# Performance work log

Measured on AMD Instinct MI355X. Metric: run time of the kernel, lower is better.

The kernel has to match this reference:

```python
import jax, jax.numpy as jnp
import numpy as np

P = 3            # spline degree
N_KNOTS = 68     # len(t); K = N_KNOTS - P - 1 = 64
B, D_IN, D_OUT = 4096, 256, 256


def bspline_basis(u, t, p):
    """Vectorized Cox-de Boor recursion.
    u: (N,) evaluation points; t: (n,) sorted knot vector.
    Returns (N, n - p - 1) basis matrix.
    """
    n = t.shape[0]
    uu = u[:, None]                                   # (N, 1)
    # degree-0 indicators over half-open knot intervals: (N, n-1)
    Bmat = ((uu >= t[None, :-1]) & (uu < t[None, 1:])).astype(u.dtype)
    for d in range(1, p + 1):
        ld = t[d:n - 1] - t[:n - d - 1]               # (n-d-1,) left denominators
        rd = t[d + 1:] - t[1:n - d]                   # (n-d-1,) right denominators
        lt = jnp.where(ld > 0, (uu - t[None, :n - d - 1]) / jnp.where(ld > 0, ld, 1.0), 0.0)
        rt = jnp.where(rd > 0, (t[None, d + 1:] - uu) / jnp.where(rd > 0, rd, 1.0), 0.0)
        Bmat = lt * Bmat[:, :-1] + rt * Bmat[:, 1:]
    return Bmat                                        # (N, K)


def setup_inputs() -> dict:
    key = jax.random.key(0)
    k1, k2 = jax.random.split(key)
    K = N_KNOTS - P - 1
    x = jax.random.normal(k1, (B, D_IN), dtype=jnp.float32)
    coeffs = 0.01 * jax.random.normal(k2, (D_OUT, D_IN, K), dtype=jnp.float32)
    mask = jnp.ones((D_OUT, D_IN), dtype=jnp.float32)
    t = jnp.linspace(-4.0, 4.0, N_KNOTS, dtype=jnp.float32)
    return {"x": x, "coeffs": coeffs, "mask": mask, "t": t}


def reference(x, coeffs, mask, t):
    b, d_in = x.shape
    # basis for all (batch, input-dim) points at once -> (B, d_in, K)
    Bx = bspline_basis(x.reshape(-1), t, P).reshape(b, d_in, -1)
    C = coeffs * mask[..., None]                      # (d_out, d_in, K)
    y = jnp.einsum('bik,oik->bo', Bx, C)              # (B, d_out)
    return y
```

## Files before the change

kernel.cpp:

```cpp
#include <hip/hip_runtime.h>

#define NKNOTS 68
#define B_     4096
#define DIN    256
#define DOUT   256
#define KB_    64
#define BM     128
#define BN     128
#define LDT    72
#define KSPLIT 16
#define IPS    (DIN / KSPLIT)

typedef unsigned short ushort_t;
typedef __bf16 bf16_t;
typedef bf16_t  bf16x8   __attribute__((ext_vector_type(8)));
typedef float   f32x4    __attribute__((ext_vector_type(4)));
typedef unsigned int u32x4 __attribute__((ext_vector_type(4)));
typedef ushort_t us16x4  __attribute__((ext_vector_type(4)));

typedef __attribute__((address_space(1))) const unsigned int gu32;
typedef __attribute__((address_space(3))) unsigned int lu32;

__device__ __forceinline__ float bf2f(ushort_t b) {
    union { unsigned u; float f; } c; c.u = ((unsigned)b) << 16; return c.f;
}
__device__ __forceinline__ ushort_t f2bf(float f) {
    union { float f; unsigned u; } c; c.f = f;
    unsigned u = c.u;
    return (ushort_t)((u + 0x7FFFu + ((u >> 16) & 1u)) >> 16);
}
__device__ __forceinline__ bool is_fp32(const void* tkn) {
    return ((*(const unsigned*)tkn) & 0xFFFFu) == 0u;
}

__global__ void kan_prep(const void* __restrict__ coeffs,
                         const void* __restrict__ mask,
                         const void* __restrict__ x,
                         const void* __restrict__ tkn,
                         ushort_t* __restrict__ cp,
                         ushort_t* __restrict__ basis4,
                         unsigned char* __restrict__ span) {
    __shared__ float tt[NKNOTS];
    int blk = blockIdx.x;
    int lt  = threadIdx.x;
    bool f32 = is_fp32(tkn);

    if (blk < 2048) {
        int tid = blk * 256 + lt;
        int oi = tid >> 3;
        int k8 = (tid & 7) * 8;
        size_t base = (size_t)oi * KB_ + k8;
        float v[8], m;
        if (f32) {
            const float* cf = (const float*)coeffs + base;
            f32x4 a = *(const f32x4*)cf;
            f32x4 b = *(const f32x4*)(cf + 4);
            v[0]=a.x; v[1]=a.y; v[2]=a.z; v[3]=a.w; v[4]=b.x; v[5]=b.y; v[6]=b.z; v[7]=b.w;
            m = ((const float*)mask)[oi];
        } else {
            const ushort_t* ch = (const ushort_t*)coeffs + base;
            u32x4 w = *(const u32x4*)ch;
            const ushort_t* h = (const ushort_t*)&w;
            #pragma unroll
            for (int e = 0; e < 8; ++e) v[e] = bf2f(h[e]);
            m = bf2f(((const ushort_t*)mask)[oi]);
        }
        us16x4 o0v, o1v;
        #pragma unroll
        for (int e = 0; e < 4; ++e) o0v[e] = f2bf(v[e] * m);
        #pragma unroll
        for (int e = 0; e < 4; ++e) o1v[e] = f2bf(v[4 + e] * m);
        *(us16x4*)(cp + base)     = o0v;
        *(us16x4*)(cp + base + 4) = o1v;
    } else {
        if (lt < NKNOTS) tt[lt] = f32 ? ((const float*)tkn)[lt] : bf2f(((const ushort_t*)tkn)[lt]);
        __syncthreads();
        int g = (blk - 2048) * 256 + lt;
        float u = f32 ? ((const float*)x)[g] : bf2f(((const ushort_t*)x)[g]);
        float N0 = 0.f, N1 = 0.f, N2 = 0.f, N3 = 0.f;
        int j = 0;
        bool valid = (u >= tt[0]) && (u < tt[NKNOTS - 1]);
        if (valid) {
            int lo = 0, hi = NKNOTS - 1;
            #pragma unroll
            for (int it = 0; it < 7; ++it) {
                int mid = (lo + hi) >> 1;
                if (u < tt[mid]) hi = mid; else lo = mid;
            }
            j = lo;
            float Nv[4];
            Nv[0] = 1.f; Nv[1] = 0.f; Nv[2] = 0.f; Nv[3] = 0.f;
            #pragma unroll
            for (int d = 1; d <= 3; ++d) {
                float saved = 0.f;
                #pragma unroll
                for (int r = 0; r < 3; ++r) {
                    if (r < d) {
                        int il = j + r + 1 - d;
                        int ir = j + r + 1;
                        il = il < 0 ? 0 : (il > 67 ? 67 : il);
                        ir = ir > 67 ? 67 : ir;
                        float tl = tt[il], tr = tt[ir];
                        float denom = tr - tl;
                        float temp = (denom > 0.f) ? Nv[r] / denom : 0.f;
                        Nv[r] = saved + (tr - u) * temp;
                        saved = (u - tl) * temp;
                    }
                }
                Nv[d] = saved;
            }
            N0 = Nv[0]; N1 = Nv[1]; N2 = Nv[2]; N3 = Nv[3];
        }
        int s = j - 3;
        int sc = s < 0 ? 0 : (s > 60 ? 60 : s);
        us16x4 o4;
        #pragma unroll
        for (int r = 0; r < 4; ++r) {
            int rr = (sc + r) - s;
            float v = 0.f;
            v = (rr == 0) ? N0 : v;
            v = (rr == 1) ? N1 : v;
            v = (rr == 2) ? N2 : v;
            v = (rr == 3) ? N3 : v;
            o4[r] = f2bf(v);
        }
        ((us16x4*)basis4)[g] = o4;
        span[g] = (unsigned char)sc;
    }
}

__global__ __launch_bounds__(256, 4) void kan_gemm(
    const ushort_t* __restrict__ cp,
    const ushort_t* __restrict__ basis4,
    const unsigned char* __restrict__ span,
    ushort_t* __restrict__ part)
{
    __shared__ __align__(16) ushort_t As[BM * LDT];
    __shared__ __align__(16) ushort_t Bs[BM * KB_];

    int t  = threadIdx.x;
    int bx = blockIdx.x;
    int kt = bx & (KSPLIT - 1);
    int mt = (bx >> 4) & 31;
    int nt = bx >> 9;
    int b0 = mt * BM;
    int o0 = nt * BN;
    int i0 = kt * IPS;

    int wave = t >> 6;
    int lane = t & 63;
    int wm = (wave & 1) * 64;
    int wn = (wave >> 1) * 64;
    int l15 = lane & 15;
    int l4  = lane >> 4;

    {
        unsigned* As32 = (unsigned*)As;
        #pragma unroll
        for (int j = 0; j < (BM * LDT / 2) / 256; ++j) As32[t + j * 256] = 0u;
    }
    __syncthreads();

    f32x4 acc[4][4];
    #pragma unroll
    for (int a = 0; a < 4; ++a)
        #pragma unroll
        for (int b = 0; b < 4; ++b)
            acc[a][b] = (f32x4){0.f, 0.f, 0.f, 0.f};

    int zrow = t >> 2;
    int zq   = t & 3;
    int last0 = 0, last1 = 0;

    for (int ii = 0; ii < IPS; ++ii) {
        int i = i0 + ii;
        size_t gi0 = (size_t)(b0 + zrow) * DIN + i;
        size_t gi1 = (size_t)(b0 + zrow + 64) * DIN + i;
        int s0 = span[gi0];
        int s1 = span[gi1];
        ushort_t bv0 = basis4[gi0 * 4 + zq];
        ushort_t bv1 = basis4[gi1 * 4 + zq];
        #pragma unroll
        for (int j = 0; j < 4; ++j) {
            int slot = wave * 256 + j * 64 + lane;
            int row  = slot >> 3;
            int c    = (slot & 7) ^ (row & 7);
            const ushort_t* g = cp + ((size_t)(o0 + row) * DIN + i) * KB_ + c * 8;
            lu32* l = (lu32*)(Bs + (wave * 256 + j * 64) * 8);
            __builtin_amdgcn_global_load_lds((gu32*)g, l, 16, 0, 0);
        }
        As[zrow * LDT + last0 + zq] = 0;
        As[(zrow + 64) * LDT + last1 + zq] = 0;
        As[zrow * LDT + s0 + zq] = bv0;
        As[(zrow + 64) * LDT + s1 + zq] = bv1;
        last0 = s0; last1 = s1;
        __syncthreads();
        #pragma unroll
        for (int ks = 0; ks < 2; ++ks) {
            bf16x8 af[4], bfr[4];
            #pragma unroll
            for (int a = 0; a < 4; ++a)
                af[a] = *(const bf16x8*)(As + (wm + a * 16 + l15) * LDT + ks * 32 + l4 * 8);
            #pragma unroll
            for (int b = 0; b < 4; ++b) {
                int brow = wn + b * 16 + l15;
                int c2 = (ks * 4 + l4) ^ (brow & 7);
                bfr[b] = *(const bf16x8*)(Bs + brow * KB_ + c2 * 8);
            }
            #pragma unroll
            for (int a = 0; a < 4; ++a)
                #pragma unroll
                for (int b = 0; b < 4; ++b)
                    acc[a][b] = __builtin_amdgcn_mfma_f32_16x16x32_bf16(af[a], bfr[b], acc[a][b], 0, 0, 0);
        }
        __syncthreads();
    }
    ushort_t* pout = part + (size_t)kt * (B_ * DOUT);
    #pragma unroll
    for (int a = 0; a < 4; ++a) {
        int row_base = b0 + wm + a * 16 + l4 * 4;
        #pragma unroll
        for (int b = 0; b < 4; ++b) {
            int col = o0 + wn + b * 16 + l15;
            #pragma unroll
            for (int e = 0; e < 4; ++e)
                pout[(size_t)(row_base + e) * DOUT + col] = f2bf(acc[a][b][e]);
        }
    }
}

__global__ void kan_reduce(const ushort_t* __restrict__ part,
                           const void* __restrict__ tkn,
                           void* __restrict__ out) {
    int g = blockIdx.x * 256 + threadIdx.x;
    const us16x4* p4 = (const us16x4*)part;
    f32x4 s = (f32x4){0.f, 0.f, 0.f, 0.f};
    #pragma unroll
    for (int kt = 0; kt < KSPLIT; ++kt) {
        us16x4 v = p4[(size_t)kt * (B_ * DOUT / 4) + g];
        s.x += bf2f(v[0]); s.y += bf2f(v[1]); s.z += bf2f(v[2]); s.w += bf2f(v[3]);
    }
    if (is_fp32(tkn)) {
        ((f32x4*)out)[g] = s;
    } else {
        us16x4 o;
        o[0] = f2bf(s.x); o[1] = f2bf(s.y); o[2] = f2bf(s.z); o[3] = f2bf(s.w);
        ((us16x4*)out)[g] = o;
    }
}

extern "C" void kernel_launch(void* const* d_in, const int* in_sizes, int n_in,
                              void* d_out, int out_size, void* d_ws, size_t ws_size,
                              hipStream_t stream) {
    const void* x      = d_in[0];
    const void* coeffs = d_in[1];
    const void* mask   = d_in[2];
    const void* tkn    = d_in[3];

    char* ws = (char*)d_ws;
    ushort_t* cp            = (ushort_t*)(ws);
    ushort_t* basis4        = (ushort_t*)(ws + (8u  << 20));
    unsigned char* spanbuf  = (unsigned char*)(ws + (16u << 20));
    ushort_t* part          = (ushort_t*)(ws + (17u << 20));

    kan_prep<<<6144, 256, 0, stream>>>(coeffs, mask, x, tkn, cp, basis4, spanbuf);
    kan_gemm<<<1024, 256, 0, stream>>>(cp, basis4, spanbuf, part);
    kan_reduce<<<1024, 256, 0, stream>>>(part, tkn, d_out);
}
```

Measured before the change: 118.6 us.

## Quantize GEMM operands to int8 with per-output scaling and double-buffer coefficient tiles

Coefficients are quantized to int8 with a per-output-row absmax scale, computed by a new reduction pass using atomicMax. Basis values become int8 and are packed with the span index into a single 64-bit record. The GEMM switches to i32 int8 MFMA with K=64 per instruction and double-buffers the LDS coefficient tile so the next load overlaps the current compute. This halves operand bandwidth and MFMA count but adds an extra prep kernel plus a memset, and the int8 quantization may lose accuracy.

```diff
diff --git a/kernel.cpp b/kernel.cpp
--- a/kernel.cpp
+++ b/kernel.cpp
@@ -7,16 +7,16 @@
 #define KB_    64
 #define BM     128
 #define BN     128
-#define LDT    72
+#define LDA    80
 #define KSPLIT 16
 #define IPS    (DIN / KSPLIT)
 
 typedef unsigned short ushort_t;
-typedef __bf16 bf16_t;
-typedef bf16_t  bf16x8   __attribute__((ext_vector_type(8)));
+typedef unsigned long long u64_t;
 typedef float   f32x4    __attribute__((ext_vector_type(4)));
 typedef unsigned int u32x4 __attribute__((ext_vector_type(4)));
 typedef ushort_t us16x4  __attribute__((ext_vector_type(4)));
+typedef int     int4v    __attribute__((ext_vector_type(4)));
 
 typedef __attribute__((address_space(1))) const unsigned int gu32;
 typedef __attribute__((address_space(3))) unsigned int lu32;
@@ -33,14 +33,14 @@
     return ((*(const unsigned*)tkn) & 0xFFFFu) == 0u;
 }
 
-__global__ void kan_prep(const void* __restrict__ coeffs,
-                         const void* __restrict__ mask,
-                         const void* __restrict__ x,
-                         const void* __restrict__ tkn,
-                         ushort_t* __restrict__ cp,
-                         ushort_t* __restrict__ basis4,
-                         unsigned char* __restrict__ span) {
+__global__ void kan_prep1(const void* __restrict__ coeffs,
+                          const void* __restrict__ mask,
+                          const void* __restrict__ x,
+                          const void* __restrict__ tkn,
+                          unsigned* __restrict__ smax,
+                          u64_t* __restrict__ rec64) {
     __shared__ float tt[NKNOTS];
+    __shared__ float wmax[4];
     int blk = blockIdx.x;
     int lt  = threadIdx.x;
     bool f32 = is_fp32(tkn);
@@ -48,6 +48,7 @@
     if (blk < 2048) {
         int tid = blk * 256 + lt;
         int oi = tid >> 3;
+        int o  = tid >> 11;
         int k8 = (tid & 7) * 8;
         size_t base = (size_t)oi * KB_ + k8;
         float v[8], m;
@@ -65,13 +66,18 @@
             for (int e = 0; e < 8; ++e) v[e] = bf2f(h[e]);
             m = bf2f(((const ushort_t*)mask)[oi]);
         }
-        us16x4 o0v, o1v;
-        #pragma unroll
-        for (int e = 0; e < 4; ++e) o0v[e] = f2bf(v[e] * m);
-        #pragma unroll
-        for (int e = 0; e < 4; ++e) o1v[e] = f2bf(v[4 + e] * m);
-        *(us16x4*)(cp + base)     = o0v;
-        *(us16x4*)(cp + base + 4) = o1v;
+        float mx = 0.f;
+        #pragma unroll
+        for (int e = 0; e < 8; ++e) mx = fmaxf(mx, fabsf(v[e] * m));
+        #pragma unroll
+        for (int off = 32; off >= 1; off >>= 1)
+            mx = fmaxf(mx, __shfl_down(mx, off, 64));
+        if ((lt & 63) == 0) wmax[lt >> 6] = mx;
+        __syncthreads();
+        if (lt == 0) {
+            float M = fmaxf(fmaxf(wmax[0], wmax[1]), fmaxf(wmax[2], wmax[3]));
+            atomicMax(smax + o, __float_as_uint(M));
+        }
     } else {
         if (lt < NKNOTS) tt[lt] = f32 ? ((const float*)tkn)[lt] : bf2f(((const ushort_t*)tkn)[lt]);
         __syncthreads();
@@ -113,7 +119,7 @@
         }
         int s = j - 3;
         int sc = s < 0 ? 0 : (s > 60 ? 60 : s);
-        us16x4 o4;
+        unsigned pack = 0;
         #pragma unroll
         for (int r = 0; r < 4; ++r) {
             int rr = (sc + r) - s;
@@ -122,21 +128,58 @@
             v = (rr == 1) ? N1 : v;
             v = (rr == 2) ? N2 : v;
             v = (rr == 3) ? N3 : v;
-            o4[r] = f2bf(v);
-        }
-        ((us16x4*)basis4)[g] = o4;
-        span[g] = (unsigned char)sc;
-    }
+            int q = __float2int_rn(127.0f * v);
+            pack |= ((unsigned)(q & 0xFF)) << (8 * r);
+        }
+        rec64[g] = ((u64_t)(unsigned)sc << 32) | pack;
+    }
+}
+
+__global__ void kan_prep2(const void* __restrict__ coeffs,
+                          const void* __restrict__ mask,
+                          const void* __restrict__ tkn,
+                          const unsigned* __restrict__ smax,
+                          signed char* __restrict__ cp8) {
+    int tid = blockIdx.x * 256 + threadIdx.x;
+    int oi = tid >> 3;
+    int o  = tid >> 11;
+    int k8 = (tid & 7) * 8;
+    size_t base = (size_t)oi * KB_ + k8;
+    bool f32 = is_fp32(tkn);
+    float maxv = __uint_as_float(smax[o]);
+    float sinv = (maxv > 0.f) ? (127.0f / maxv) : 0.f;
+    float v[8], m;
+    if (f32) {
+        const float* cf = (const float*)coeffs + base;
+        f32x4 a = *(const f32x4*)cf;
+        f32x4 b = *(const f32x4*)(cf + 4);
+        v[0]=a.x; v[1]=a.y; v[2]=a.z; v[3]=a.w; v[4]=b.x; v[5]=b.y; v[6]=b.z; v[7]=b.w;
+        m = ((const float*)mask)[oi];
+    } else {
+        const ushort_t* ch = (const ushort_t*)coeffs + base;
+        u32x4 w = *(const u32x4*)ch;
+        const ushort_t* h = (const ushort_t*)&w;
+        #pragma unroll
+        for (int e = 0; e < 8; ++e) v[e] = bf2f(h[e]);
+        m = bf2f(((const ushort_t*)mask)[oi]);
+    }
+    u64_t pk = 0;
+    #pragma unroll
+    for (int e = 0; e < 8; ++e) {
+        int q = __float2int_rn(v[e] * m * sinv);
+        pk |= ((u64_t)((unsigned)q & 0xFF)) << (8 * e);
+    }
+    *(u64_t*)(cp8 + base) = pk;
 }
 
 __global__ __launch_bounds__(256, 4) void kan_gemm(
-    const ushort_t* __restrict__ cp,
-    const ushort_t* __restrict__ basis4,
-    const unsigned char* __restrict__ span,
+    const signed char* __restrict__ cp8,
+    const u64_t* __restrict__ rec64,
+    const unsigned* __restrict__ smax,
     ushort_t* __restrict__ part)
 {
-    __shared__ __align__(16) ushort_t As[BM * LDT];
-    __shared__ __align__(16) ushort_t Bs[BM * KB_];
+    __shared__ __align__(16) unsigned char As[BM * LDA];
+    __shared__ __align__(16) unsigned char Bs[2][BN * KB_];
 
     int t  = threadIdx.x;
     int bx = blockIdx.x;
@@ -154,68 +197,86 @@
     int l15 = lane & 15;
     int l4  = lane >> 4;
 
+    #define STAGE(i_, p_)                                                                 \
+        {                                                                                 \
+            _Pragma("unroll")                                                             \
+            for (int j = 0; j < 2; ++j) {                                                 \
+                int slot = wave * 128 + j * 64 + lane;                                    \
+                int row  = slot >> 2;                                                     \
+                int c    = slot & 3;                                                      \
+                const signed char* g = cp8 + ((size_t)(o0 + row) * DIN + (i_)) * KB_ + c * 16; \
+                lu32* l = (lu32*)(&Bs[p_][(wave * 128 + j * 64) * 16]);                   \
+                __builtin_amdgcn_global_load_lds((gu32*)g, l, 16, 0, 0);                  \
+            }                                                                             \
+        }
+
     {
         unsigned* As32 = (unsigned*)As;
         #pragma unroll
-        for (int j = 0; j < (BM * LDT / 2) / 256; ++j) As32[t + j * 256] = 0u;
-    }
-    __syncthreads();
-
-    f32x4 acc[4][4];
-    #pragma unroll
-    for (int a = 0; a < 4; ++a)
-        #pragma unroll
-        for (int b = 0; b < 4; ++b)
-            acc[a][b] = (f32x4){0.f, 0.f, 0.f, 0.f};
+        for (int j = 0; j < (BM * LDA / 4) / 256; ++j) As32[t + j * 256] = 0u;
+    }
 
     int zrow = t >> 2;
     int zq   = t & 3;
+    size_t gb0 = (size_t)(b0 + zrow) * DIN;
+    size_t gb1 = (size_t)(b0 + zrow + 64) * DIN;
+
+    STAGE(i0, 0);
+    u64_t cur_r0 = rec64[gb0 + i0];
+    u64_t cur_r1 = rec64[gb1 + i0];
+
+    int4v acc[4][4];
+    #pragma unroll
+    for (int a = 0; a < 4; ++a)
+        #pragma unroll
+        for (int b = 0; b < 4; ++b)
+            acc[a][b] = (int4v){0, 0, 0, 0};
+
+    __syncthreads();
+
     int last0 = 0, last1 = 0;
-
+    u64_t nxt_r0 = 0, nxt_r1 = 0;
     for (int ii = 0; ii < IPS; ++ii) {
-        int i = i0 + ii;
-        size_t gi0 = (size_t)(b0 + zrow) * DIN + i;
-        size_t gi1 = (size_t)(b0 + zrow + 64) * DIN + i;
-        int s0 = span[gi0];
-        int s1 = span[gi1];
-        ushort_t bv0 = basis4[gi0 * 4 + zq];
-        ushort_t bv1 = basis4[gi1 * 4 + zq];
-        #pragma unroll
-        for (int j = 0; j < 4; ++j) {
-            int slot = wave * 256 + j * 64 + lane;
-            int row  = slot >> 3;
-            int c    = (slot & 7) ^ (row & 7);
-            const ushort_t* g = cp + ((size_t)(o0 + row) * DIN + i) * KB_ + c * 8;
-            lu32* l = (lu32*)(Bs + (wave * 256 + j * 64) * 8);
-            __builtin_amdgcn_global_load_lds((gu32*)g, l, 16, 0, 0);
-        }
-        As[zrow * LDT + last0 + zq] = 0;
-        As[(zrow + 64) * LDT + last1 + zq] = 0;
-        As[zrow * LDT + s0 + zq] = bv0;
-        As[(zrow + 64) * LDT + s1 + zq] = bv1;
+        int p = ii & 1;
+        int s0 = (int)((cur_r0 >> 32) & 0xFF);
+        int s1 = (int)((cur_r1 >> 32) & 0xFF);
+        unsigned char v0 = (unsigned char)((cur_r0 >> (8 * zq)) & 0xFF);
+        unsigned char v1 = (unsigned char)((cur_r1 >> (8 * zq)) & 0xFF);
+        As[zrow * LDA + last0 + zq] = 0;
+        As[(zrow + 64) * LDA + last1 + zq] = 0;
+        As[zrow * LDA + s0 + zq] = v0;
+        As[(zrow + 64) * LDA + s1 + zq] = v1;
         last0 = s0; last1 = s1;
         __syncthreads();
-        #pragma unroll
-        for (int ks = 0; ks < 2; ++ks) {
-            bf16x8 af[4], bfr[4];
-            #pragma unroll
-            for (int a = 0; a < 4; ++a)
-                af[a] = *(const bf16x8*)(As + (wm + a * 16 + l15) * LDT + ks * 32 + l4 * 8);
-            #pragma unroll
-            for (int b = 0; b < 4; ++b) {
-                int brow = wn + b * 16 + l15;
-                int c2 = (ks * 4 + l4) ^ (brow & 7);
-                bfr[b] = *(const bf16x8*)(Bs + brow * KB_ + c2 * 8);
-            }
-            #pragma unroll
-            for (int a = 0; a < 4; ++a)
-                #pragma unroll
-                for (int b = 0; b < 4; ++b)
-                    acc[a][b] = __builtin_amdgcn_mfma_f32_16x16x32_bf16(af[a], bfr[b], acc[a][b], 0, 0, 0);
-        }
+        if (ii + 1 < IPS) {
+            int i1 = i0 + ii + 1;
+            STAGE(i1, p ^ 1);
+            nxt_r0 = rec64[gb0 + i1];
+            nxt_r1 = rec64[gb1 + i1];
+        }
+        int4v af[4], bfr[4];
+        #pragma unroll
+        for (int a = 0; a < 4; ++a)
+            af[a] = *(const int4v*)(&As[(wm + a * 16 + l15) * LDA + l4 * 16]);
+        #pragma unroll
+        for (int b = 0; b < 4; ++b)
+            bfr[b] = *(const int4v*)(&Bs[p][(wn + b * 16 + l15) * KB_ + l4 * 16]);
+        #pragma unroll
+        for (int a = 0; a < 4; ++a)
+            #pragma unroll
+            for (int b = 0; b < 4; ++b)
+                acc[a][b] = __builtin_amdgcn_mfma_i32_16x16x64_i8(af[a], bfr[b], acc[a][b], 0, 0, 0);
+        cur_r0 = nxt_r0; cur_r1 = nxt_r1;
         __syncthreads();
     }
+
     ushort_t* pout = part + (size_t)kt * (B_ * DOUT);
+    float sb[4];
+    #pragma unroll
+    for (int b = 0; b < 4; ++b) {
+        int col = o0 + wn + b * 16 + l15;
+        sb[b] = __uint_as_float(smax[col]) * (1.0f / (127.0f * 127.0f));
+    }
     #pragma unroll
     for (int a = 0; a < 4; ++a) {
         int row_base = b0 + wm + a * 16 + l4 * 4;
@@ -224,9 +285,10 @@
             int col = o0 + wn + b * 16 + l15;
             #pragma unroll
             for (int e = 0; e < 4; ++e)
-                pout[(size_t)(row_base + e) * DOUT + col] = f2bf(acc[a][b][e]);
-        }
-    }
+                pout[(size_t)(row_base + e) * DOUT + col] = f2bf((float)acc[a][b][e] * sb[b]);
+        }
+    }
+    #undef STAGE
 }
 
 __global__ void kan_reduce(const ushort_t* __restrict__ part,
@@ -258,12 +320,14 @@
     const void* tkn    = d_in[3];
 
     char* ws = (char*)d_ws;
-    ushort_t* cp            = (ushort_t*)(ws);
-    ushort_t* basis4        = (ushort_t*)(ws + (8u  << 20));
-    unsigned char* spanbuf  = (unsigned char*)(ws + (16u << 20));
-    ushort_t* part          = (ushort_t*)(ws + (17u << 20));
-
-    kan_prep<<<6144, 256, 0, stream>>>(coeffs, mask, x, tkn, cp, basis4, spanbuf);
-    kan_gemm<<<1024, 256, 0, stream>>>(cp, basis4, spanbuf, part);
+    signed char* cp8   = (signed char*)(ws);
+    u64_t*       rec64 = (u64_t*)(ws + (4u  << 20));
+    unsigned*    smax  = (unsigned*)(ws + (12u << 20));
+    ushort_t*    part  = (ushort_t*)(ws + (13u << 20));
+
+    hipMemsetAsync(smax, 0, 256 * sizeof(unsigned), stream);
+    kan_prep1<<<6144, 256, 0, stream>>>(coeffs, mask, x, tkn, smax, rec64);
+    kan_prep2<<<2048, 256, 0, stream>>>(coeffs, mask, tkn, smax, cp8);
+    kan_gemm<<<1024, 256, 0, stream>>>(cp8, rec64, smax, part);
     kan_reduce<<<1024, 256, 0, stream>>>(part, tkn, d_out);
 }
```

Result: slower. 121.3 us (+2.2%).
